# Optimization experiments

Hardware: AMD Instinct MI355X
Metric: run time of the kernel (lower is better)

## Reference

```python
import jax, jax.numpy as jnp
import numpy as np

NSTEP = 5  # mean-field iterations (module default)


def setup_inputs() -> dict:
    key = jax.random.key(0)
    k1, k2 = jax.random.split(key)
    N = 4096  # number of 'person' constants
    return {
        "logits_smoke": jax.random.normal(k1, (N, 2), dtype=jnp.float32),
        "logits_friend": jax.random.normal(k2, (N, N, 2), dtype=jnp.float32),
        "weights": jnp.ones((1,), dtype=jnp.float32) * 5.0,  # rule weight param
    }


def _mp_step(base_s, base_f, cur_s, cur_f, weights):
    # q-values via softmax over labels
    qs = jax.nn.softmax(cur_s, axis=-1)   # [N, 2]
    qf = jax.nn.softmax(cur_f, axis=-1)   # [N, N, 2]
    # per-atom 'unsatisfied' factors: 1 - sum(q * vals)
    # neg atom (vals=[1,0]) -> q[...,1]; pos atom (vals=[0,1]) -> q[...,0]
    s1 = qs[:, 1]        # !smoke(a) factor
    s0 = qs[:, 0]        # smoke(b) factor
    f1 = qf[:, :, 1]     # !friend(a,b) factor
    w0 = weights[0]
    # message to smoke(a) (neg target -> label 0): einsum 'ab,b->a'
    m_s0 = (f1 @ s0) * w0                      # [N]
    # message to smoke(b) (pos target -> label 1): einsum 'a,ab->b'
    m_s1 = (s1 @ f1) * w0                      # [N]
    # message to friend(a,b) (neg target -> label 0): einsum 'a,b->ab'
    m_f0 = (s1[:, None] * s0[None, :]) * w0    # [N, N]
    msg_s = jnp.stack([m_s0, m_s1], axis=-1)                   # [N, 2]
    msg_f = jnp.stack([m_f0, jnp.zeros_like(m_f0)], axis=-1)   # [N, N, 2]
    return base_s + msg_s, base_f + msg_f


def reference(logits_smoke, logits_friend, weights):
    cur_s, cur_f = logits_smoke, logits_friend
    for _ in range(NSTEP):
        cur_s, cur_f = _mp_step(logits_smoke, logits_friend, cur_s, cur_f, weights)
    return cur_s, cur_f
```

## Files before the change

### kernel.cpp

```cpp
#include <hip/hip_runtime.h>
#include <hip/hip_fp16.h>

#define NN 4096
constexpr int TPB = 256;
constexpr int NSTRIP = 2;
constexpr int CPB = 2048;
constexpr int RPB = 8;
constexpr int NROWG = NN / RPB;
constexpr int NRSLOT = NSTRIP * (TPB / 64);
constexpr int NBLK = NSTRIP * NROWG;

typedef float    f32x4 __attribute__((ext_vector_type(4)));
typedef _Float16 f16x8 __attribute__((ext_vector_type(8)));

__device__ __forceinline__ float sigmoidf_(float x) {
    return 1.0f / (1.0f + __expf(-x));
}

template <int MODE>
__global__ __launch_bounds__(TPB) void pass_kernel(
    const float2* __restrict__ bs, const f32x4* __restrict__ bf,
    f16x8* __restrict__ df, f32x4* __restrict__ of,
    const float* __restrict__ s1c, const float* __restrict__ s1p,
    const float* __restrict__ wptr,
    float* __restrict__ rowpart, float* __restrict__ colpart,
    float* __restrict__ s1store) {
    const int t = threadIdx.x;
    const int bid = blockIdx.x;
    const int strip = bid & (NSTRIP - 1);
    const int rg = bid >> 1;
    const int j0 = strip * CPB + t * 8;
    const int i0 = rg * RPB;
    const float w = wptr[0];

    float s0cv[8], ws0p[8];
#pragma unroll
    for (int k = 0; k < 8; ++k) {
        if (MODE <= 1) {
            float2 v = bs[j0 + k];
            s0cv[k] = 1.0f - sigmoidf_(v.y - v.x);
            ws0p[k] = 0.0f;
        } else {
            s0cv[k] = 1.0f - s1c[j0 + k];
            ws0p[k] = w * (1.0f - s1p[j0 + k]);
        }
    }
    if (MODE <= 1) {
        if (bid < NN / TPB) {
            int x = bid * TPB + t;
            float2 v = bs[x];
            s1store[x] = sigmoidf_(v.y - v.x);
        }
    }
    float colacc[8] = {0.f, 0.f, 0.f, 0.f, 0.f, 0.f, 0.f, 0.f};

#pragma unroll 2
    for (int r = 0; r < RPB; ++r) {
        const int i = i0 + r;
        float s1ci, s1pi;
        if (MODE <= 1) {
            float2 v = bs[i];
            s1ci = sigmoidf_(v.y - v.x);
            s1pi = 0.0f;
        } else {
            s1ci = s1c[i];
            s1pi = s1p[i];
        }
        float dd[8];
        if (MODE == 2) {
            f16x8 h = df[((size_t)i * NN + j0) >> 3];
#pragma unroll
            for (int k = 0; k < 8; ++k) dd[k] = (float)h[k];
        } else {
            const size_t u = ((size_t)i * NN + j0) >> 1;
            f32x4 v0 = bf[u], v1 = bf[u + 1], v2 = bf[u + 2], v3 = bf[u + 3];
            dd[0] = v0.y - v0.x; dd[1] = v0.w - v0.z;
            dd[2] = v1.y - v1.x; dd[3] = v1.w - v1.z;
            dd[4] = v2.y - v2.x; dd[5] = v2.w - v2.z;
            dd[6] = v3.y - v3.x; dd[7] = v3.w - v3.z;
            if (MODE == 0) {
                f16x8 h;
#pragma unroll
                for (int k = 0; k < 8; ++k) h[k] = (_Float16)dd[k];
                df[((size_t)i * NN + j0) >> 3] = h;
            }
            if (MODE == 4) {
                const float wi = w * s1ci;
                of[u]     = f32x4{v0.x + wi * s0cv[0], v0.y, v0.z + wi * s0cv[1], v0.w};
                of[u + 1] = f32x4{v1.x + wi * s0cv[2], v1.y, v1.z + wi * s0cv[3], v1.w};
                of[u + 2] = f32x4{v2.x + wi * s0cv[4], v2.y, v2.z + wi * s0cv[5], v2.w};
                of[u + 3] = f32x4{v3.x + wi * s0cv[6], v3.y, v3.z + wi * s0cv[7], v3.w};
            }
        }
        float rowp = 0.f;
#pragma unroll
        for (int k = 0; k < 8; ++k) {
            float f1 = sigmoidf_(dd[k] - s1pi * ws0p[k]);
            colacc[k] += s1ci * f1;
            rowp += f1 * s0cv[k];
        }
#pragma unroll
        for (int off = 32; off > 0; off >>= 1) rowp += __shfl_down(rowp, off);
        if ((t & 63) == 0)
            rowpart[(size_t)(strip * (TPB / 64) + (t >> 6)) * NN + i] = rowp;
    }
    float* cp = colpart + (size_t)rg * NN + j0;
    *reinterpret_cast<f32x4*>(cp) = f32x4{colacc[0], colacc[1], colacc[2], colacc[3]};
    *reinterpret_cast<f32x4*>(cp + 4) = f32x4{colacc[4], colacc[5], colacc[6], colacc[7]};
}

__global__ __launch_bounds__(1024) void update_kernel(
    const float* __restrict__ rowpart, const float* __restrict__ colpart,
    const float2* __restrict__ bs, const float* __restrict__ wptr,
    float* __restrict__ s1next, float2* __restrict__ out_s, int writeOut) {
    __shared__ float red0[16][64];
    __shared__ float red1[16][64];
    const int col = threadIdx.x & 63;
    const int sl = threadIdx.x >> 6;
    const int x = blockIdx.x * 64 + col;

    float acc1 = 0.f;
    const int g0 = sl * (NROWG / 16);
#pragma unroll 8
    for (int g = g0; g < g0 + NROWG / 16; ++g) acc1 += colpart[(size_t)g * NN + x];
    red1[sl][col] = acc1;
    red0[sl][col] = (sl < NRSLOT) ? rowpart[(size_t)sl * NN + x] : 0.f;
    __syncthreads();
    if (sl == 0) {
        float m0 = 0.f, m1 = 0.f;
#pragma unroll
        for (int s = 0; s < 16; ++s) {
            m0 += red0[s][col];
            m1 += red1[s][col];
        }
        float w = wptr[0];
        float2 b = bs[x];
        float c0 = b.x + w * m0;
        float c1 = b.y + w * m1;
        if (writeOut) out_s[x] = make_float2(c0, c1);
        else s1next[x] = sigmoidf_(c1 - c0);
    }
}

extern "C" void kernel_launch(void* const* d_in, const int* in_sizes, int n_in,
                              void* d_out, int out_size, void* d_ws,
                              size_t ws_size, hipStream_t stream) {
    const float2* bs = (const float2*)d_in[0];
    const f32x4* bf = (const f32x4*)d_in[1];
    const float* wptr = (const float*)d_in[2];
    float2* out_s = (float2*)d_out;
    f32x4* out_f = (f32x4*)((float*)d_out + 2 * NN);

    char* ws = (char*)d_ws;
    size_t off = 0;
    auto alloc = [&](size_t bytes) {
        void* p = ws + off;
        off = (off + bytes + 255) & ~(size_t)255;
        return p;
    };
    float* sa = (float*)alloc((size_t)NN * 4);
    float* sb = (float*)alloc((size_t)NN * 4);
    float* sc = (float*)alloc((size_t)NN * 4);
    float* rowpart = (float*)alloc((size_t)NRSLOT * NN * 4);
    float* colpart = (float*)alloc((size_t)NROWG * NN * 4);
    f16x8* df = (f16x8*)(ws + off);
    const bool use_df = (ws_size >= off + (size_t)NN * NN * 2);

    const dim3 gP(NBLK), bP(TPB);
    const dim3 gU(NN / 64), bU(1024);

    if (use_df)
        pass_kernel<0><<<gP, bP, 0, stream>>>(bs, bf, df, nullptr, nullptr,
                                              nullptr, wptr, rowpart, colpart, sa);
    else
        pass_kernel<1><<<gP, bP, 0, stream>>>(bs, bf, df, nullptr, nullptr,
                                              nullptr, wptr, rowpart, colpart, sa);
    update_kernel<<<gU, bU, 0, stream>>>(rowpart, colpart, bs, wptr, sb, nullptr, 0);

    if (use_df) {
        pass_kernel<2><<<gP, bP, 0, stream>>>(bs, bf, df, nullptr, sb, sa, wptr,
                                              rowpart, colpart, nullptr);
        update_kernel<<<gU, bU, 0, stream>>>(rowpart, colpart, bs, wptr, sc, nullptr, 0);
        pass_kernel<2><<<gP, bP, 0, stream>>>(bs, bf, df, nullptr, sc, sb, wptr,
                                              rowpart, colpart, nullptr);
        update_kernel<<<gU, bU, 0, stream>>>(rowpart, colpart, bs, wptr, sa, nullptr, 0);
        pass_kernel<2><<<gP, bP, 0, stream>>>(bs, bf, df, nullptr, sa, sc, wptr,
                                              rowpart, colpart, nullptr);
        update_kernel<<<gU, bU, 0, stream>>>(rowpart, colpart, bs, wptr, sb, nullptr, 0);
    } else {
        pass_kernel<3><<<gP, bP, 0, stream>>>(bs, bf, df, nullptr, sb, sa, wptr,
                                              rowpart, colpart, nullptr);
        update_kernel<<<gU, bU, 0, stream>>>(rowpart, colpart, bs, wptr, sc, nullptr, 0);
        pass_kernel<3><<<gP, bP, 0, stream>>>(bs, bf, df, nullptr, sc, sb, wptr,
                                              rowpart, colpart, nullptr);
        update_kernel<<<gU, bU, 0, stream>>>(rowpart, colpart, bs, wptr, sa, nullptr, 0);
        pass_kernel<3><<<gP, bP, 0, stream>>>(bs, bf, df, nullptr, sa, sc, wptr,
                                              rowpart, colpart, nullptr);
        update_kernel<<<gU, bU, 0, stream>>>(rowpart, colpart, bs, wptr, sb, nullptr, 0);
    }
    pass_kernel<4><<<gP, bP, 0, stream>>>(bs, bf, df, out_f, sb, sa, wptr,
                                          rowpart, colpart, nullptr);
    update_kernel<<<gU, bU, 0, stream>>>(rowpart, colpart, bs, wptr, nullptr, out_s, 1);
}
```

Measured before the change: 150.8 us.

## Use 2D tiles and fold the update reduction into each pass prologue

Replaces the row-strip pass layout with 128x128 tiles, which cuts the number of column partials per step from 512 to 32. Each pass kernel now reduces the previous step's row and column partials itself, for both the current and the prior step, so the separate update kernel launches go away. A small final kernel writes the smoke output. This trades redundant partial-sum reads in every block, 64 strided loads per thread per step, for fewer launches and less partial traffic, and it adds shared-memory staging and shuffle reductions.

```diff
diff --git a/kernel.cpp b/kernel.cpp
--- a/kernel.cpp
+++ b/kernel.cpp
@@ -3,12 +3,10 @@
 
 #define NN 4096
 constexpr int TPB = 256;
-constexpr int NSTRIP = 2;
-constexpr int CPB = 2048;
-constexpr int RPB = 8;
-constexpr int NROWG = NN / RPB;
-constexpr int NRSLOT = NSTRIP * (TPB / 64);
-constexpr int NBLK = NSTRIP * NROWG;
+constexpr int TILE = 128;
+constexpr int NT = NN / TILE;
+constexpr int NBLK = NT * NT;
+constexpr int NPART = NT;
 
 typedef float    f32x4 __attribute__((ext_vector_type(4)));
 typedef _Float16 f16x8 __attribute__((ext_vector_type(8)));
@@ -17,74 +15,102 @@
     return 1.0f / (1.0f + __expf(-x));
 }
 
-template <int MODE>
+template <int STEPK, int SRC, int WDF, int EPI>
 __global__ __launch_bounds__(TPB) void pass_kernel(
     const float2* __restrict__ bs, const f32x4* __restrict__ bf,
     f16x8* __restrict__ df, f32x4* __restrict__ of,
-    const float* __restrict__ s1c, const float* __restrict__ s1p,
-    const float* __restrict__ wptr,
-    float* __restrict__ rowpart, float* __restrict__ colpart,
-    float* __restrict__ s1store) {
+    const float* __restrict__ rpC, const float* __restrict__ cpC,
+    const float* __restrict__ rpP, const float* __restrict__ cpP,
+    float* __restrict__ rpO, float* __restrict__ cpO,
+    const float* __restrict__ wptr) {
     const int t = threadIdx.x;
-    const int bid = blockIdx.x;
-    const int strip = bid & (NSTRIP - 1);
-    const int rg = bid >> 1;
-    const int j0 = strip * CPB + t * 8;
-    const int i0 = rg * RPB;
+    const int ct = blockIdx.x & (NT - 1);
+    const int rt = blockIdx.x >> 5;
+    const int j0 = ct * TILE;
+    const int i0 = rt * TILE;
     const float w = wptr[0];
 
+    __shared__ float sc_row[TILE];
+    __shared__ float sp_row[TILE];
+    __shared__ float s0c_col[TILE];
+    __shared__ float wp_col[TILE];
+    __shared__ float colred[4][TILE];
+
+    {
+        const bool isRow = (t < TILE);
+        const int x = isRow ? (i0 + t) : (j0 + (t - TILE));
+        float scur, sprev;
+        float2 b = bs[x];
+        if (STEPK == 1) {
+            scur = sigmoidf_(b.y - b.x);
+            sprev = 0.0f;
+        } else {
+            float m0 = 0.f, m1 = 0.f;
+#pragma unroll
+            for (int s = 0; s < NPART; ++s) {
+                m0 += rpC[(size_t)s * NN + x];
+                m1 += cpC[(size_t)s * NN + x];
+            }
+            scur = sigmoidf_((b.y + w * m1) - (b.x + w * m0));
+            if (STEPK == 2) {
+                sprev = sigmoidf_(b.y - b.x);
+            } else {
+                float p0 = 0.f, p1 = 0.f;
+#pragma unroll
+                for (int s = 0; s < NPART; ++s) {
+                    p0 += rpP[(size_t)s * NN + x];
+                    p1 += cpP[(size_t)s * NN + x];
+                }
+                sprev = sigmoidf_((b.y + w * p1) - (b.x + w * p0));
+            }
+        }
+        if (isRow) {
+            sc_row[t] = scur;
+            sp_row[t] = sprev;
+        } else {
+            s0c_col[t - TILE] = 1.0f - scur;
+            wp_col[t - TILE] = w * (1.0f - sprev);
+        }
+    }
+    __syncthreads();
+
+    const int c = t & 15;
+    const int rg = t >> 4;
+    const int jg = j0 + c * 8;
+
     float s0cv[8], ws0p[8];
 #pragma unroll
     for (int k = 0; k < 8; ++k) {
-        if (MODE <= 1) {
-            float2 v = bs[j0 + k];
-            s0cv[k] = 1.0f - sigmoidf_(v.y - v.x);
-            ws0p[k] = 0.0f;
-        } else {
-            s0cv[k] = 1.0f - s1c[j0 + k];
-            ws0p[k] = w * (1.0f - s1p[j0 + k]);
-        }
-    }
-    if (MODE <= 1) {
-        if (bid < NN / TPB) {
-            int x = bid * TPB + t;
-            float2 v = bs[x];
-            s1store[x] = sigmoidf_(v.y - v.x);
-        }
+        s0cv[k] = s0c_col[c * 8 + k];
+        ws0p[k] = wp_col[c * 8 + k];
     }
     float colacc[8] = {0.f, 0.f, 0.f, 0.f, 0.f, 0.f, 0.f, 0.f};
 
 #pragma unroll 2
-    for (int r = 0; r < RPB; ++r) {
-        const int i = i0 + r;
-        float s1ci, s1pi;
-        if (MODE <= 1) {
-            float2 v = bs[i];
-            s1ci = sigmoidf_(v.y - v.x);
-            s1pi = 0.0f;
-        } else {
-            s1ci = s1c[i];
-            s1pi = s1p[i];
-        }
+    for (int rr = 0; rr < 8; ++rr) {
+        const int lr = rg * 8 + rr;
+        const int i = i0 + lr;
+        const float s1ci = sc_row[lr];
+        const float s1pi = sp_row[lr];
         float dd[8];
-        if (MODE == 2) {
-            f16x8 h = df[((size_t)i * NN + j0) >> 3];
+        if (SRC == 1) {
+            f16x8 h = df[((size_t)i * NN + jg) >> 3];
 #pragma unroll
             for (int k = 0; k < 8; ++k) dd[k] = (float)h[k];
         } else {
-            const size_t u = ((size_t)i * NN + j0) >> 1;
+            const size_t u = ((size_t)i * NN + jg) >> 1;
             f32x4 v0 = bf[u], v1 = bf[u + 1], v2 = bf[u + 2], v3 = bf[u + 3];
             dd[0] = v0.y - v0.x; dd[1] = v0.w - v0.z;
             dd[2] = v1.y - v1.x; dd[3] = v1.w - v1.z;
             dd[4] = v2.y - v2.x; dd[5] = v2.w - v2.z;
             dd[6] = v3.y - v3.x; dd[7] = v3.w - v3.z;
-            if (MODE == 0) {
+            if (WDF) {
                 f16x8 h;
 #pragma unroll
                 for (int k = 0; k < 8; ++k) h[k] = (_Float16)dd[k];
-                df[((size_t)i * NN + j0) >> 3] = h;
-            }
-            if (MODE == 4) {
+                df[((size_t)i * NN + jg) >> 3] = h;
+            }
+            if (EPI) {
                 const float wi = w * s1ci;
                 of[u]     = f32x4{v0.x + wi * s0cv[0], v0.y, v0.z + wi * s0cv[1], v0.w};
                 of[u + 1] = f32x4{v1.x + wi * s0cv[2], v1.y, v1.z + wi * s0cv[3], v1.w};
@@ -99,47 +125,44 @@
             colacc[k] += s1ci * f1;
             rowp += f1 * s0cv[k];
         }
-#pragma unroll
-        for (int off = 32; off > 0; off >>= 1) rowp += __shfl_down(rowp, off);
-        if ((t & 63) == 0)
-            rowpart[(size_t)(strip * (TPB / 64) + (t >> 6)) * NN + i] = rowp;
-    }
-    float* cp = colpart + (size_t)rg * NN + j0;
-    *reinterpret_cast<f32x4*>(cp) = f32x4{colacc[0], colacc[1], colacc[2], colacc[3]};
-    *reinterpret_cast<f32x4*>(cp + 4) = f32x4{colacc[4], colacc[5], colacc[6], colacc[7]};
-}
-
-__global__ __launch_bounds__(1024) void update_kernel(
-    const float* __restrict__ rowpart, const float* __restrict__ colpart,
-    const float2* __restrict__ bs, const float* __restrict__ wptr,
-    float* __restrict__ s1next, float2* __restrict__ out_s, int writeOut) {
-    __shared__ float red0[16][64];
-    __shared__ float red1[16][64];
-    const int col = threadIdx.x & 63;
-    const int sl = threadIdx.x >> 6;
-    const int x = blockIdx.x * 64 + col;
-
-    float acc1 = 0.f;
-    const int g0 = sl * (NROWG / 16);
-#pragma unroll 8
-    for (int g = g0; g < g0 + NROWG / 16; ++g) acc1 += colpart[(size_t)g * NN + x];
-    red1[sl][col] = acc1;
-    red0[sl][col] = (sl < NRSLOT) ? rowpart[(size_t)sl * NN + x] : 0.f;
+        rowp += __shfl_xor(rowp, 1);
+        rowp += __shfl_xor(rowp, 2);
+        rowp += __shfl_xor(rowp, 4);
+        rowp += __shfl_xor(rowp, 8);
+        if (c == 0) rpO[(size_t)ct * NN + i] = rowp;
+    }
+
+#pragma unroll
+    for (int k = 0; k < 8; ++k) {
+        colacc[k] += __shfl_xor(colacc[k], 16);
+        colacc[k] += __shfl_xor(colacc[k], 32);
+    }
+    const int wv = t >> 6;
+    if ((t & 48) == 0) {
+#pragma unroll
+        for (int k = 0; k < 8; ++k) colred[wv][c * 8 + k] = colacc[k];
+    }
     __syncthreads();
-    if (sl == 0) {
-        float m0 = 0.f, m1 = 0.f;
-#pragma unroll
-        for (int s = 0; s < 16; ++s) {
-            m0 += red0[s][col];
-            m1 += red1[s][col];
-        }
-        float w = wptr[0];
-        float2 b = bs[x];
-        float c0 = b.x + w * m0;
-        float c1 = b.y + w * m1;
-        if (writeOut) out_s[x] = make_float2(c0, c1);
-        else s1next[x] = sigmoidf_(c1 - c0);
-    }
+    if (t < TILE) {
+        float v = colred[0][t] + colred[1][t] + colred[2][t] + colred[3][t];
+        cpO[(size_t)rt * NN + j0 + t] = v;
+    }
+}
+
+__global__ __launch_bounds__(256) void outs_kernel(
+    const float2* __restrict__ bs, const float* __restrict__ rp5,
+    const float* __restrict__ cp5, const float* __restrict__ wptr,
+    float2* __restrict__ out_s) {
+    const int x = blockIdx.x * 256 + threadIdx.x;
+    float m0 = 0.f, m1 = 0.f;
+#pragma unroll
+    for (int s = 0; s < NPART; ++s) {
+        m0 += rp5[(size_t)s * NN + x];
+        m1 += cp5[(size_t)s * NN + x];
+    }
+    const float w = wptr[0];
+    float2 b = bs[x];
+    out_s[x] = make_float2(b.x + w * m0, b.y + w * m1);
 }
 
 extern "C" void kernel_launch(void* const* d_in, const int* in_sizes, int n_in,
@@ -158,47 +181,42 @@
         off = (off + bytes + 255) & ~(size_t)255;
         return p;
     };
-    float* sa = (float*)alloc((size_t)NN * 4);
-    float* sb = (float*)alloc((size_t)NN * 4);
-    float* sc = (float*)alloc((size_t)NN * 4);
-    float* rowpart = (float*)alloc((size_t)NRSLOT * NN * 4);
-    float* colpart = (float*)alloc((size_t)NROWG * NN * 4);
+    const size_t PSZ = (size_t)NPART * NN;
+    float* P0 = (float*)alloc(2 * PSZ * 4);
+    float* P1 = (float*)alloc(2 * PSZ * 4);
+    float* P2 = (float*)alloc(2 * PSZ * 4);
     f16x8* df = (f16x8*)(ws + off);
     const bool use_df = (ws_size >= off + (size_t)NN * NN * 2);
 
+    auto rp = [&](float* P) { return P; };
+    auto cp = [&](float* P) { return P + PSZ; };
+
     const dim3 gP(NBLK), bP(TPB);
-    const dim3 gU(NN / 64), bU(1024);
+    const float* nil = nullptr;
 
     if (use_df)
-        pass_kernel<0><<<gP, bP, 0, stream>>>(bs, bf, df, nullptr, nullptr,
-                                              nullptr, wptr, rowpart, colpart, sa);
+        pass_kernel<1, 0, 1, 0><<<gP, bP, 0, stream>>>(
+            bs, bf, df, nullptr, nil, nil, nil, nil, rp(P0), cp(P0), wptr);
     else
-        pass_kernel<1><<<gP, bP, 0, stream>>>(bs, bf, df, nullptr, nullptr,
-                                              nullptr, wptr, rowpart, colpart, sa);
-    update_kernel<<<gU, bU, 0, stream>>>(rowpart, colpart, bs, wptr, sb, nullptr, 0);
+        pass_kernel<1, 0, 0, 0><<<gP, bP, 0, stream>>>(
+            bs, bf, df, nullptr, nil, nil, nil, nil, rp(P0), cp(P0), wptr);
 
     if (use_df) {
-        pass_kernel<2><<<gP, bP, 0, stream>>>(bs, bf, df, nullptr, sb, sa, wptr,
-                                              rowpart, colpart, nullptr);
-        update_kernel<<<gU, bU, 0, stream>>>(rowpart, colpart, bs, wptr, sc, nullptr, 0);
-        pass_kernel<2><<<gP, bP, 0, stream>>>(bs, bf, df, nullptr, sc, sb, wptr,
-                                              rowpart, colpart, nullptr);
-        update_kernel<<<gU, bU, 0, stream>>>(rowpart, colpart, bs, wptr, sa, nullptr, 0);
-        pass_kernel<2><<<gP, bP, 0, stream>>>(bs, bf, df, nullptr, sa, sc, wptr,
-                                              rowpart, colpart, nullptr);
-        update_kernel<<<gU, bU, 0, stream>>>(rowpart, colpart, bs, wptr, sb, nullptr, 0);
+        pass_kernel<2, 1, 0, 0><<<gP, bP, 0, stream>>>(
+            bs, bf, df, nullptr, rp(P0), cp(P0), nil, nil, rp(P1), cp(P1), wptr);
+        pass_kernel<3, 1, 0, 0><<<gP, bP, 0, stream>>>(
+            bs, bf, df, nullptr, rp(P1), cp(P1), rp(P0), cp(P0), rp(P2), cp(P2), wptr);
+        pass_kernel<3, 1, 0, 0><<<gP, bP, 0, stream>>>(
+            bs, bf, df, nullptr, rp(P2), cp(P2), rp(P1), cp(P1), rp(P0), cp(P0), wptr);
     } else {
-        pass_kernel<3><<<gP, bP, 0, stream>>>(bs, bf, df, nullptr, sb, sa, wptr,
-                                              rowpart, colpart, nullptr);
-        update_kernel<<<gU, bU, 0, stream>>>(rowpart, colpart, bs, wptr, sc, nullptr, 0);
-        pass_kernel<3><<<gP, bP, 0, stream>>>(bs, bf, df, nullptr, sc, sb, wptr,
-                                              rowpart, colpart, nullptr);
-        update_kernel<<<gU, bU, 0, stream>>>(rowpart, colpart, bs, wptr, sa, nullptr, 0);
-        pass_kernel<3><<<gP, bP, 0, stream>>>(bs, bf, df, nullptr, sa, sc, wptr,
-                                              rowpart, colpart, nullptr);
-        update_kernel<<<gU, bU, 0, stream>>>(rowpart, colpart, bs, wptr, sb, nullptr, 0);
-    }
-    pass_kernel<4><<<gP, bP, 0, stream>>>(bs, bf, df, out_f, sb, sa, wptr,
-                                          rowpart, colpart, nullptr);
-    update_kernel<<<gU, bU, 0, stream>>>(rowpart, colpart, bs, wptr, nullptr, out_s, 1);
-}
+        pass_kernel<2, 0, 0, 0><<<gP, bP, 0, stream>>>(
+            bs, bf, df, nullptr, rp(P0), cp(P0), nil, nil, rp(P1), cp(P1), wptr);
+        pass_kernel<3, 0, 0, 0><<<gP, bP, 0, stream>>>(
+            bs, bf, df, nullptr, rp(P1), cp(P1), rp(P0), cp(P0), rp(P2), cp(P2), wptr);
+        pass_kernel<3, 0, 0, 0><<<gP, bP, 0, stream>>>(
+            bs, bf, df, nullptr, rp(P2), cp(P2), rp(P1), cp(P1), rp(P0), cp(P0), wptr);
+    }
+    pass_kernel<3, 0, 0, 1><<<gP, bP, 0, stream>>>(
+        bs, bf, df, out_f, rp(P0), cp(P0), rp(P2), cp(P2), rp(P1), cp(P1), wptr);
+    outs_kernel<<<NN / 256, 256, 0, stream>>>(bs, rp(P1), cp(P1), wptr, out_s);
+}
```

Result: slower. 210.4 us (+39.6%).

## Prefetch final-pass friend logits into cache during fp16 passes; halve rows per block

Applied to the files above, without the earlier changes.

During the three MODE 2 passes, each thread issues one dummy load per 128-byte line of the original fp32 friend-logit tensor, splitting the tensor into thirds across the passes. The intent is to warm the last-level cache so the final MODE 4 pass, which must re-read the full fp32 tensor, sees fewer DRAM misses. Rows per block are also cut from 8 to 4 and the row loop is fully unrolled, which doubles the grid and the colpart partial-sum buffer that update_kernel reduces. The prefetch adds extra memory traffic to the bandwidth-bound passes and only helps if the lines survive in the MALL until the last pass.

```diff
diff --git a/kernel.cpp b/kernel.cpp
--- a/kernel.cpp
+++ b/kernel.cpp
@@ -5,10 +5,11 @@
 constexpr int TPB = 256;
 constexpr int NSTRIP = 2;
 constexpr int CPB = 2048;
-constexpr int RPB = 8;
+constexpr int RPB = 4;
 constexpr int NROWG = NN / RPB;
 constexpr int NRSLOT = NSTRIP * (TPB / 64);
 constexpr int NBLK = NSTRIP * NROWG;
+constexpr unsigned BF_LINES = 1048576u;
 
 typedef float    f32x4 __attribute__((ext_vector_type(4)));
 typedef _Float16 f16x8 __attribute__((ext_vector_type(8)));
@@ -24,7 +25,7 @@
     const float* __restrict__ s1c, const float* __restrict__ s1p,
     const float* __restrict__ wptr,
     float* __restrict__ rowpart, float* __restrict__ colpart,
-    float* __restrict__ s1store) {
+    float* __restrict__ s1store, int pf) {
     const int t = threadIdx.x;
     const int bid = blockIdx.x;
     const int strip = bid & (NSTRIP - 1);
@@ -32,6 +33,14 @@
     const int j0 = strip * CPB + t * 8;
     const int i0 = rg * RPB;
     const float w = wptr[0];
+
+    float pfv = 0.0f;
+    if (MODE == 2) {
+        const unsigned b0 = (BF_LINES * (unsigned)pf) / 3u;
+        const unsigned b1 = (BF_LINES * (unsigned)(pf + 1)) / 3u;
+        const unsigned line = b0 + (unsigned)bid * TPB + (unsigned)t;
+        if (line < b1) pfv = reinterpret_cast<const float*>(bf)[(size_t)line * 32];
+    }
 
     float s0cv[8], ws0p[8];
 #pragma unroll
@@ -54,7 +63,7 @@
     }
     float colacc[8] = {0.f, 0.f, 0.f, 0.f, 0.f, 0.f, 0.f, 0.f};
 
-#pragma unroll 2
+#pragma unroll
     for (int r = 0; r < RPB; ++r) {
         const int i = i0 + r;
         float s1ci, s1pi;
@@ -107,6 +116,8 @@
     float* cp = colpart + (size_t)rg * NN + j0;
     *reinterpret_cast<f32x4*>(cp) = f32x4{colacc[0], colacc[1], colacc[2], colacc[3]};
     *reinterpret_cast<f32x4*>(cp + 4) = f32x4{colacc[4], colacc[5], colacc[6], colacc[7]};
+
+    if (MODE == 2) asm volatile("" : : "v"(pfv));
 }
 
 __global__ __launch_bounds__(1024) void update_kernel(
@@ -171,34 +182,34 @@
 
     if (use_df)
         pass_kernel<0><<<gP, bP, 0, stream>>>(bs, bf, df, nullptr, nullptr,
-                                              nullptr, wptr, rowpart, colpart, sa);
+                                              nullptr, wptr, rowpart, colpart, sa, -1);
     else
         pass_kernel<1><<<gP, bP, 0, stream>>>(bs, bf, df, nullptr, nullptr,
-                                              nullptr, wptr, rowpart, colpart, sa);
+                                              nullptr, wptr, rowpart, colpart, sa, -1);
     update_kernel<<<gU, bU, 0, stream>>>(rowpart, colpart, bs, wptr, sb, nullptr, 0);
 
     if (use_df) {
         pass_kernel<2><<<gP, bP, 0, stream>>>(bs, bf, df, nullptr, sb, sa, wptr,
-                                              rowpart, colpart, nullptr);
+                                              rowpart, colpart, nullptr, 0);
         update_kernel<<<gU, bU, 0, stream>>>(rowpart, colpart, bs, wptr, sc, nullptr, 0);
         pass_kernel<2><<<gP, bP, 0, stream>>>(bs, bf, df, nullptr, sc, sb, wptr,
-                                              rowpart, colpart, nullptr);
+                                              rowpart, colpart, nullptr, 1);
         update_kernel<<<gU, bU, 0, stream>>>(rowpart, colpart, bs, wptr, sa, nullptr, 0);
         pass_kernel<2><<<gP, bP, 0, stream>>>(bs, bf, df, nullptr, sa, sc, wptr,
-                                              rowpart, colpart, nullptr);
+                                              rowpart, colpart, nullptr, 2);
         update_kernel<<<gU, bU, 0, stream>>>(rowpart, colpart, bs, wptr, sb, nullptr, 0);
     } else {
         pass_kernel<3><<<gP, bP, 0, stream>>>(bs, bf, df, nullptr, sb, sa, wptr,
-                                              rowpart, colpart, nullptr);
+                                              rowpart, colpart, nullptr, -1);
         update_kernel<<<gU, bU, 0, stream>>>(rowpart, colpart, bs, wptr, sc, nullptr, 0);
         pass_kernel<3><<<gP, bP, 0, stream>>>(bs, bf, df, nullptr, sc, sb, wptr,
-                                              rowpart, colpart, nullptr);
+                                              rowpart, colpart, nullptr, -1);
         update_kernel<<<gU, bU, 0, stream>>>(rowpart, colpart, bs, wptr, sa, nullptr, 0);
         pass_kernel<3><<<gP, bP, 0, stream>>>(bs, bf, df, nullptr, sa, sc, wptr,
-                                              rowpart, colpart, nullptr);
+                                              rowpart, colpart, nullptr, -1);
         update_kernel<<<gU, bU, 0, stream>>>(rowpart, colpart, bs, wptr, sb, nullptr, 0);
     }
     pass_kernel<4><<<gP, bP, 0, stream>>>(bs, bf, df, out_f, sb, sa, wptr,
-                                          rowpart, colpart, nullptr);
+                                          rowpart, colpart, nullptr, -1);
     update_kernel<<<gU, bU, 0, stream>>>(rowpart, colpart, bs, wptr, nullptr, out_s, 1);
 }
```

Result: slower. 187.7 us (+24.5%).
